# Performance work log

Measured on AMD Instinct MI355X. Metric: run time of the kernel, lower is better.

## Reference

```python
import jax, jax.numpy as jnp
import numpy as np

N, E, H, L, G = 50000, 500000, 128, 4, 1000
EPS = 1e-7      # GENConv message eps
LN_EPS = 1e-5   # torch LayerNorm default


def setup_inputs() -> dict:
    key = jax.random.key(0)
    ks = jax.random.split(key, 24)
    d = {}
    d["x"] = jax.random.normal(ks[0], (N, 9), jnp.float32)
    d["edge_index"] = jax.random.randint(ks[1], (2, E), 0, N, jnp.int32)
    d["edge_attr"] = jax.random.normal(ks[2], (E, 3), jnp.float32)
    d["batch"] = jnp.sort(jax.random.randint(ks[3], (N,), 0, G, jnp.int32))
    s9, s3, sh, s2h = 1/np.sqrt(9), 1/np.sqrt(3), 1/np.sqrt(H), 1/np.sqrt(2*H)
    u = lambda k, shp, s: jax.random.uniform(k, shp, jnp.float32, -s, s)
    d["enc_node_W"] = u(ks[4], (9, H), s9)
    d["enc_node_b"] = u(ks[5], (H,), s9)
    d["enc_edge_W"] = u(ks[6], (3, H), s3)
    d["enc_edge_b"] = u(ks[7], (H,), s3)
    d["ln_g"] = jnp.ones((L, H), jnp.float32)   # DeepGCNLayer pre-norm affine
    d["ln_b"] = jnp.zeros((L, H), jnp.float32)
    d["W1"] = u(ks[8], (L, H, 2*H), sh)          # GENConv MLP layer 1
    d["b1"] = u(ks[9], (L, 2*H), sh)
    d["mlp_ln_g"] = jnp.ones((L, 2*H), jnp.float32)
    d["mlp_ln_b"] = jnp.zeros((L, 2*H), jnp.float32)
    d["W2"] = u(ks[10], (L, 2*H, H), s2h)        # GENConv MLP layer 2
    d["b2"] = u(ks[11], (L, H), s2h)
    d["t"] = jnp.ones((L,), jnp.float32)         # learnable softmax temperature, init 1.0
    return d


def layernorm(x, g, b):
    mu = x.mean(-1, keepdims=True)
    var = ((x - mu) ** 2).mean(-1, keepdims=True)
    return (x - mu) / jnp.sqrt(var + LN_EPS) * g + b


def genconv(h, src, dst, ea, t, W1, b1, lg, lb, W2, b2):
    # message: relu(x_j + edge_attr) + eps   -> [E, H]
    msg = jax.nn.relu(h[src] + ea) + EPS
    # softmax aggregation over incoming edges, per channel
    logits = t * msg
    m = jax.ops.segment_max(logits, dst, num_segments=N)
    num = jnp.exp(logits - m[dst])
    den = jax.ops.segment_sum(num, dst, num_segments=N)
    alpha = num / den[dst]
    agg = jax.ops.segment_sum(msg * alpha, dst, num_segments=N)
    out = agg + h  # root residual inside GENConv
    z = jax.nn.relu(layernorm(out @ W1 + b1, lg, lb))
    return z @ W2 + b2


def reference(x, edge_index, edge_attr, batch, enc_node_W, enc_node_b,
              enc_edge_W, enc_edge_b, ln_g, ln_b, W1, b1, mlp_ln_g, mlp_ln_b,
              W2, b2, t):
    src, dst = edge_index[0], edge_index[1]
    h = x @ enc_node_W + enc_node_b            # node encoder  [N, H]
    ea = edge_attr @ enc_edge_W + enc_edge_b   # edge encoder  [E, H]
    # layer 0: conv only (DeeperGCN forward uses layers[0].conv directly)
    h = genconv(h, src, dst, ea, t[0], W1[0], b1[0], mlp_ln_g[0], mlp_ln_b[0], W2[0], b2[0])
    # layers 1..L-1: res+ block: x + conv(relu(LN(x))); dropout is identity (eval)
    for i in range(1, L):
        z = jax.nn.relu(layernorm(h, ln_g[i], ln_b[i]))
        h = h + genconv(z, src, dst, ea, t[i], W1[i], b1[i], mlp_ln_g[i], mlp_ln_b[i], W2[i], b2[i])
    h = jax.nn.relu(layernorm(h, ln_g[0], ln_b[0]))  # reuses layer-0 norm
    # global mean pool over graphs
    counts = jax.ops.segment_sum(jnp.ones((N,), h.dtype), batch, num_segments=G)
    sums = jax.ops.segment_sum(h, batch, num_segments=G)
    return sums / jnp.maximum(counts, 1.0)[:, None]
```

## Files before the change

### kernel.cpp

```cpp
#include <hip/hip_runtime.h>

#define NN 50000
#define NE 500000
#define HD 128
#define HD2 256
#define NL 4
#define NG 1000

constexpr float MSG_EPS = 1e-7f;
constexpr float LNEPS   = 1e-5f;

typedef float  f32x4  __attribute__((ext_vector_type(4)));
typedef __bf16 bf16x8 __attribute__((ext_vector_type(8)));

__device__ __forceinline__ unsigned short f2b(float f) {
    unsigned int u = __float_as_uint(f);
    unsigned int r = u + 0x7FFFu + ((u >> 16) & 1u);
    return (unsigned short)(r >> 16);
}
__device__ __forceinline__ float b2f(unsigned short h) {
    return __uint_as_float(((unsigned int)h) << 16);
}
__device__ __forceinline__ unsigned int pack2(float a, float b) {
    return (unsigned int)f2b(a) | ((unsigned int)f2b(b) << 16);
}

__global__ void k_encode_nodes(const float* __restrict__ x, const float* __restrict__ W,
                               const float* __restrict__ b, unsigned short* __restrict__ zb) {
    int n = blockIdx.x;
    int c = threadIdx.x;
    float xr[9];
#pragma unroll
    for (int k = 0; k < 9; k++) xr[k] = x[n * 9 + k];
    float acc = b[c];
#pragma unroll
    for (int k = 0; k < 9; k++) acc = fmaf(xr[k], W[k * HD + c], acc);
    zb[n * HD + c] = f2b(acc);
}

__global__ void k_prep(const float* __restrict__ W1, const float* __restrict__ W2,
                       unsigned short* __restrict__ W1T, unsigned short* __restrict__ W2T) {
    int idx = blockIdx.x * 256 + threadIdx.x;
    {
        int k = idx & 127, n = (idx >> 7) & 255, l = idx >> 15;
        W1T[idx] = f2b(W1[(l * 128 + k) * 256 + n]);
    }
    {
        int k = idx & 255, n = (idx >> 8) & 127, l = idx >> 15;
        W2T[idx] = f2b(W2[(l * 256 + k) * 128 + n]);
    }
}

__global__ void k_hist(const int* __restrict__ dst, int* __restrict__ counts) {
    int e = blockIdx.x * blockDim.x + threadIdx.x;
    if (e < NE) atomicAdd(&counts[dst[e]], 1);
}

#define SCAN_B 512
__global__ void k_scan1(const int* __restrict__ counts, int* __restrict__ incl,
                        int* __restrict__ bsum) {
    __shared__ int s[SCAN_B];
    int i = blockIdx.x * SCAN_B + threadIdx.x;
    int v = (i < NN) ? counts[i] : 0;
    s[threadIdx.x] = v;
    __syncthreads();
    for (int off = 1; off < SCAN_B; off <<= 1) {
        int t = (threadIdx.x >= off) ? s[threadIdx.x - off] : 0;
        __syncthreads();
        s[threadIdx.x] += t;
        __syncthreads();
    }
    if (i < NN) incl[i] = s[threadIdx.x];
    if (threadIdx.x == SCAN_B - 1) bsum[blockIdx.x] = s[threadIdx.x];
}

__global__ void k_scan2(const int* __restrict__ bsum, int* __restrict__ boff, int nb) {
    __shared__ int s[128];
    int v = (threadIdx.x < nb) ? bsum[threadIdx.x] : 0;
    s[threadIdx.x] = v;
    __syncthreads();
    for (int off = 1; off < 128; off <<= 1) {
        int t = (threadIdx.x >= off) ? s[threadIdx.x - off] : 0;
        __syncthreads();
        s[threadIdx.x] += t;
        __syncthreads();
    }
    if (threadIdx.x < nb) boff[threadIdx.x] = s[threadIdx.x] - v;
}

__global__ void k_scan3(const int* __restrict__ incl, const int* __restrict__ boff,
                        int* __restrict__ row_start) {
    int i = blockIdx.x * SCAN_B + threadIdx.x;
    if (i < NN) row_start[i + 1] = incl[i] + boff[blockIdx.x];
    if (i == 0) row_start[0] = 0;
}

__global__ void k_scatter(const int* __restrict__ src, const int* __restrict__ dst,
                          const float* __restrict__ eattr, const int* __restrict__ row_start,
                          int* __restrict__ cursor, float4* __restrict__ aperm) {
    int e = blockIdx.x * blockDim.x + threadIdx.x;
    if (e >= NE) return;
    int d = dst[e];
    int p = row_start[d] + atomicAdd(&cursor[d], 1);
    float4 v;
    v.x = eattr[e * 3 + 0];
    v.y = eattr[e * 3 + 1];
    v.z = eattr[e * 3 + 2];
    v.w = __int_as_float(src[e]);
    aperm[p] = v;
}

__device__ __forceinline__ void edge_acc2(float4 a, unsigned int zz, float2 w0, float2 w1,
                                          float2 w2, float2 bb, float tv, float& num0,
                                          float& num1, float& wm0, float& wm1) {
    float zx = b2f((unsigned short)zz), zy = b2f((unsigned short)(zz >> 16));
    float eax = fmaf(a.x, w0.x, fmaf(a.y, w1.x, fmaf(a.z, w2.x, bb.x)));
    float eay = fmaf(a.x, w0.y, fmaf(a.y, w1.y, fmaf(a.z, w2.y, bb.y)));
    float mx = fmaxf(zx + eax, 0.f) + MSG_EPS;
    float my = fmaxf(zy + eay, 0.f) + MSG_EPS;
    float ex = __expf(tv * mx), ey = __expf(tv * my);
    num0 += ex;
    num1 += ey;
    wm0 = fmaf(mx, ex, wm0);
    wm1 = fmaf(my, ey, wm1);
}

#define AGG_CHUNKS_R ((((NN + 31) / 32) + 7) / 8 * 8)
#define AGG_BLOCKS (AGG_CHUNKS_R * 8)
__global__ __launch_bounds__(256) void k_aggregate(const unsigned short* __restrict__ zbin,
                                                   const float4* __restrict__ aperm,
                                                   const int* __restrict__ row_start,
                                                   const float* __restrict__ We,
                                                   const float* __restrict__ be,
                                                   const float* __restrict__ t, int layer,
                                                   unsigned int* __restrict__ outb) {
    int w = threadIdx.x >> 6, lane = threadIdx.x & 63;
    int bid = blockIdx.x;
    int jj = bid >> 3;
    int chunk = (bid & 7) + ((jj >> 3) << 3);
    int n = chunk * 32 + (jj & 7) * 4 + w;
    if (n >= NN) return;
    int c = lane * 2;
    float2 w0 = *(const float2*)&We[c];
    float2 w1 = *(const float2*)&We[HD + c];
    float2 w2 = *(const float2*)&We[2 * HD + c];
    float2 bb = *(const float2*)&be[c];
    float tv = t[layer];
    int s0 = row_start[n], s1 = row_start[n + 1];
    float num0 = 0.f, num1 = 0.f, wm0 = 0.f, wm1 = 0.f;
    const unsigned int* z32 = (const unsigned int*)zbin;
    int p = s0;
    for (; p + 4 <= s1; p += 4) {
        float4 a0 = aperm[p], a1 = aperm[p + 1], a2 = aperm[p + 2], a3 = aperm[p + 3];
        unsigned int zz0 = z32[(size_t)__float_as_int(a0.w) * 64 + lane];
        unsigned int zz1 = z32[(size_t)__float_as_int(a1.w) * 64 + lane];
        unsigned int zz2 = z32[(size_t)__float_as_int(a2.w) * 64 + lane];
        unsigned int zz3 = z32[(size_t)__float_as_int(a3.w) * 64 + lane];
        edge_acc2(a0, zz0, w0, w1, w2, bb, tv, num0, num1, wm0, wm1);
        edge_acc2(a1, zz1, w0, w1, w2, bb, tv, num0, num1, wm0, wm1);
        edge_acc2(a2, zz2, w0, w1, w2, bb, tv, num0, num1, wm0, wm1);
        edge_acc2(a3, zz3, w0, w1, w2, bb, tv, num0, num1, wm0, wm1);
    }
    for (; p < s1; p++) {
        float4 a = aperm[p];
        unsigned int zz = z32[(size_t)__float_as_int(a.w) * 64 + lane];
        edge_acc2(a, zz, w0, w1, w2, bb, tv, num0, num1, wm0, wm1);
    }
    unsigned int zn = z32[(size_t)n * 64 + lane];
    float ox = ((s1 > s0) ? (wm0 / num0) : 0.f) + b2f((unsigned short)zn);
    float oy = ((s1 > s0) ? (wm1 / num1) : 0.f) + b2f((unsigned short)(zn >> 16));
    outb[(size_t)n * 64 + lane] = pack2(ox, oy);
}

#define BM 32
#define HS_LD 264
#define HT_LD 136

__global__ __launch_bounds__(256) void k_mlp(const unsigned short* __restrict__ outb,
                                             const unsigned short* __restrict__ W1T,
                                             const float* __restrict__ b1l,
                                             const float* __restrict__ lgl,
                                             const float* __restrict__ lbl,
                                             const unsigned short* __restrict__ W2T,
                                             const float* __restrict__ b2l,
                                             unsigned short* __restrict__ h,
                                             const float* __restrict__ gn,
                                             const float* __restrict__ bn,
                                             unsigned short* __restrict__ zb,
                                             int add_residual, int store_h) {
    __shared__ __align__(16) unsigned short Hs[BM * HS_LD];
    __shared__ __align__(16) unsigned short Ht[BM * HT_LD];
    __shared__ __align__(16) float2 st1[2][16][4];

    int nb = blockIdx.x * BM;
    int tid = threadIdx.x;
    int w = tid >> 6, lane = tid & 63, q = lane >> 4, i = lane & 15;

    unsigned int hv[8];
    const unsigned int* h32c = (const unsigned int*)h;
    if (add_residual) {
#pragma unroll
        for (int it = 0; it < 8; it++) {
            int row = nb + w + it * 4;
            hv[it] = (row < NN) ? h32c[(size_t)row * 64 + lane] : 0u;
        }
    } else {
#pragma unroll
        for (int it = 0; it < 8; it++) hv[it] = 0u;
    }
    float2 gg = *(const float2*)&gn[lane * 2];
    float2 cc = *(const float2*)&bn[lane * 2];

    f32x4 acc[2][4];
#pragma unroll
    for (int rt = 0; rt < 2; rt++)
#pragma unroll
        for (int ct = 0; ct < 4; ct++) acc[rt][ct] = (f32x4){0.f, 0.f, 0.f, 0.f};

    bf16x8 acur[2], bcur[4];
#pragma unroll
    for (int rt = 0; rt < 2; rt++) {
        int row = nb + rt * 16 + i;
        acur[rt] = (row < NN) ? *(const bf16x8*)&outb[(size_t)row * HD + q * 8]
                              : (bf16x8)(__bf16)0.f;
    }
#pragma unroll
    for (int ct = 0; ct < 4; ct++)
        bcur[ct] = *(const bf16x8*)&W1T[(w * 64 + ct * 16 + i) * HD + q * 8];

#pragma unroll
    for (int ks = 0; ks < 4; ks++) {
        bf16x8 anxt[2], bnxt[4];
        if (ks < 3) {
#pragma unroll
            for (int rt = 0; rt < 2; rt++) {
                int row = nb + rt * 16 + i;
                anxt[rt] = (row < NN)
                               ? *(const bf16x8*)&outb[(size_t)row * HD + (ks + 1) * 32 + q * 8]
                               : (bf16x8)(__bf16)0.f;
            }
#pragma unroll
            for (int ct = 0; ct < 4; ct++)
                bnxt[ct] =
                    *(const bf16x8*)&W1T[(w * 64 + ct * 16 + i) * HD + (ks + 1) * 32 + q * 8];
        }
#pragma unroll
        for (int rt = 0; rt < 2; rt++)
#pragma unroll
            for (int ct = 0; ct < 4; ct++)
                acc[rt][ct] =
                    __builtin_amdgcn_mfma_f32_16x16x32_bf16(acur[rt], bcur[ct], acc[rt][ct],
                                                            0, 0, 0);
        if (ks < 3) {
#pragma unroll
            for (int rt = 0; rt < 2; rt++) acur[rt] = anxt[rt];
#pragma unroll
            for (int ct = 0; ct < 4; ct++) bcur[ct] = bnxt[ct];
        }
    }

#pragma unroll
    for (int ct = 0; ct < 4; ct++) {
        float bb = b1l[w * 64 + ct * 16 + i];
#pragma unroll
        for (int rt = 0; rt < 2; rt++)
#pragma unroll
            for (int r = 0; r < 4; r++) acc[rt][ct][r] += bb;
    }

    {
        float sv[2][4], qv[2][4];
#pragma unroll
        for (int rt = 0; rt < 2; rt++)
#pragma unroll
            for (int r = 0; r < 4; r++) {
                float s = acc[rt][0][r] + acc[rt][1][r] + acc[rt][2][r] + acc[rt][3][r];
                float sq = 0.f;
#pragma unroll
                for (int ct = 0; ct < 4; ct++) sq = fmaf(acc[rt][ct][r], acc[rt][ct][r], sq);
                sv[rt][r] = s;
                qv[rt][r] = sq;
            }
#pragma unroll
        for (int m = 1; m <= 8; m <<= 1)
#pragma unroll
            for (int rt = 0; rt < 2; rt++)
#pragma unroll
                for (int r = 0; r < 4; r++) {
                    sv[rt][r] += __shfl_xor(sv[rt][r], m);
                    qv[rt][r] += __shfl_xor(qv[rt][r], m);
                }
        if (i == 0) {
#pragma unroll
            for (int rt = 0; rt < 2; rt++)
#pragma unroll
                for (int r = 0; r < 4; r++)
                    st1[rt][q * 4 + r][w] = make_float2(sv[rt][r], qv[rt][r]);
        }
    }
    __syncthreads();

    {
        float mu[2][4], inv[2][4];
#pragma unroll
        for (int rt = 0; rt < 2; rt++)
#pragma unroll
            for (int r = 0; r < 4; r++) {
                const float4* sp = (const float4*)&st1[rt][q * 4 + r][0];
                float4 a = sp[0], b = sp[1];
                float S = a.x + a.z + b.x + b.z;
                float Q = a.y + a.w + b.y + b.w;
                float m_ = S * (1.f / 256.f);
                float v_ = Q * (1.f / 256.f) - m_ * m_;
                mu[rt][r] = m_;
                inv[rt][r] = rsqrtf(v_ + LNEPS);
            }
#pragma unroll
        for (int ct = 0; ct < 4; ct++) {
            float g = lgl[w * 64 + ct * 16 + i];
            float c = lbl[w * 64 + ct * 16 + i];
#pragma unroll
            for (int rt = 0; rt < 2; rt++)
#pragma unroll
                for (int r = 0; r < 4; r++) {
                    float v =
                        fmaxf(fmaf((acc[rt][ct][r] - mu[rt][r]) * inv[rt][r], g, c), 0.f);
                    Hs[(rt * 16 + q * 4 + r) * HS_LD + w * 64 + ct * 16 + i] = f2b(v);
                }
        }
    }
    __syncthreads();

    f32x4 acc2[2][2];
#pragma unroll
    for (int rt = 0; rt < 2; rt++)
#pragma unroll
        for (int ct = 0; ct < 2; ct++) acc2[rt][ct] = (f32x4){0.f, 0.f, 0.f, 0.f};

    bf16x8 hc[2], bc[2];
#pragma unroll
    for (int rt = 0; rt < 2; rt++) hc[rt] = *(const bf16x8*)&Hs[(rt * 16 + i) * HS_LD + q * 8];
#pragma unroll
    for (int ct = 0; ct < 2; ct++)
        bc[ct] = *(const bf16x8*)&W2T[(w * 32 + ct * 16 + i) * HD2 + q * 8];

#pragma unroll
    for (int ks = 0; ks < 8; ks++) {
        bf16x8 hn[2], bn2[2];
        if (ks < 7) {
#pragma unroll
            for (int rt = 0; rt < 2; rt++)
                hn[rt] = *(const bf16x8*)&Hs[(rt * 16 + i) * HS_LD + (ks + 1) * 32 + q * 8];
#pragma unroll
            for (int ct = 0; ct < 2; ct++)
                bn2[ct] =
                    *(const bf16x8*)&W2T[(w * 32 + ct * 16 + i) * HD2 + (ks + 1) * 32 + q * 8];
        }
#pragma unroll
        for (int rt = 0; rt < 2; rt++)
#pragma unroll
            for (int ct = 0; ct < 2; ct++)
                acc2[rt][ct] = __builtin_amdgcn_mfma_f32_16x16x32_bf16(hc[rt], bc[ct],
                                                                      acc2[rt][ct], 0, 0, 0);
        if (ks < 7) {
#pragma unroll
            for (int rt = 0; rt < 2; rt++) hc[rt] = hn[rt];
#pragma unroll
            for (int ct = 0; ct < 2; ct++) bc[ct] = bn2[ct];
        }
    }

#pragma unroll
    for (int ct = 0; ct < 2; ct++) {
        float bb = b2l[w * 32 + ct * 16 + i];
#pragma unroll
        for (int rt = 0; rt < 2; rt++)
#pragma unroll
            for (int r = 0; r < 4; r++)
                Ht[(rt * 16 + q * 4 + r) * HT_LD + w * 32 + ct * 16 + i] =
                    f2b(acc2[rt][ct][r] + bb);
    }
    __syncthreads();

    {
        const unsigned int* Ht32 = (const unsigned int*)Ht;
        unsigned int* h32 = (unsigned int*)h;
        unsigned int* zb32 = (unsigned int*)zb;
#pragma unroll
        for (int it = 0; it < 8; it++) {
            int rr = w + it * 4;
            int row = nb + rr;
            unsigned int tv = Ht32[rr * (HT_LD / 2) + lane];
            float cx = b2f((unsigned short)tv) + b2f((unsigned short)hv[it]);
            float cy = b2f((unsigned short)(tv >> 16)) + b2f((unsigned short)(hv[it] >> 16));
            float s = cx + cy, sq = cx * cx + cy * cy;
#pragma unroll
            for (int m = 32; m >= 1; m >>= 1) {
                s += __shfl_xor(s, m);
                sq += __shfl_xor(sq, m);
            }
            float mu = s * (1.f / 128.f);
            float var = sq * (1.f / 128.f) - mu * mu;
            float inv = rsqrtf(var + LNEPS);
            float z0 = fmaxf(fmaf((cx - mu) * inv, gg.x, cc.x), 0.f);
            float z1 = fmaxf(fmaf((cy - mu) * inv, gg.y, cc.y), 0.f);
            if (row < NN) {
                if (store_h) h32[(size_t)row * 64 + lane] = pack2(cx, cy);
                zb32[(size_t)row * 64 + lane] = pack2(z0, z1);
            }
        }
    }
}

__global__ void k_gbounds(const int* __restrict__ batch, int* __restrict__ gstart) {
    int g = blockIdx.x * blockDim.x + threadIdx.x;
    if (g > NG) return;
    int lo = 0, hi = NN;
    while (lo < hi) {
        int mid = (lo + hi) >> 1;
        if (batch[mid] < g) lo = mid + 1;
        else hi = mid;
    }
    gstart[g] = lo;
}

__global__ void k_pool(const unsigned short* __restrict__ zb, const int* __restrict__ gstart,
                       float* __restrict__ out) {
    int g = blockIdx.x;
    int c = threadIdx.x;
    int a = gstart[g], b = gstart[g + 1];
    float s0 = 0.f, s1 = 0.f;
    int n = a;
    for (; n + 2 <= b; n += 2) {
        s0 += b2f(zb[(size_t)n * HD + c]);
        s1 += b2f(zb[(size_t)(n + 1) * HD + c]);
    }
    if (n < b) s0 += b2f(zb[(size_t)n * HD + c]);
    out[g * HD + c] = (s0 + s1) / fmaxf((float)(b - a), 1.f);
}

extern "C" void kernel_launch(void* const* d_in, const int* in_sizes, int n_in, void* d_out,
                              int out_size, void* d_ws, size_t ws_size, hipStream_t stream) {
    const float* x     = (const float*)d_in[0];
    const int* ei      = (const int*)d_in[1];
    const float* eattr = (const float*)d_in[2];
    const int* batch   = (const int*)d_in[3];
    const float* encW  = (const float*)d_in[4];
    const float* encB  = (const float*)d_in[5];
    const float* eW    = (const float*)d_in[6];
    const float* eB    = (const float*)d_in[7];
    const float* ln_g  = (const float*)d_in[8];
    const float* ln_b  = (const float*)d_in[9];
    const float* W1    = (const float*)d_in[10];
    const float* b1    = (const float*)d_in[11];
    const float* mlg   = (const float*)d_in[12];
    const float* mlb   = (const float*)d_in[13];
    const float* W2    = (const float*)d_in[14];
    const float* b2    = (const float*)d_in[15];
    const float* t     = (const float*)d_in[16];
    const int* src = ei;
    const int* dst = ei + NE;

    char* w = (char*)d_ws;
    auto alloc = [&](size_t bytes) {
        char* p = w;
        w += (bytes + 255) & ~size_t(255);
        return p;
    };
    unsigned short* h    = (unsigned short*)alloc(sizeof(unsigned short) * NN * HD);
    unsigned short* zb   = (unsigned short*)alloc(sizeof(unsigned short) * NN * HD);
    unsigned int* outb   = (unsigned int*)alloc(sizeof(unsigned int) * NN * HD / 2);
    float4* aperm        = (float4*)alloc(sizeof(float4) * NE);
    int* row_start       = (int*)alloc(sizeof(int) * (NN + 1));
    int* counts          = (int*)alloc(sizeof(int) * NN);
    int* cursor          = (int*)alloc(sizeof(int) * NN);
    int* incl            = (int*)alloc(sizeof(int) * NN);
    int* bsum            = (int*)alloc(sizeof(int) * 128);
    int* boff            = (int*)alloc(sizeof(int) * 128);
    int* gstart          = (int*)alloc(sizeof(int) * (NG + 1));
    unsigned short* W1T  = (unsigned short*)alloc(sizeof(unsigned short) * NL * HD * HD2);
    unsigned short* W2T  = (unsigned short*)alloc(sizeof(unsigned short) * NL * HD2 * HD);

    hipMemsetAsync(counts, 0, sizeof(int) * NN, stream);
    hipMemsetAsync(cursor, 0, sizeof(int) * NN, stream);

    k_prep<<<512, 256, 0, stream>>>(W1, W2, W1T, W2T);
    k_encode_nodes<<<NN, HD, 0, stream>>>(x, encW, encB, zb);
    k_hist<<<(NE + 255) / 256, 256, 0, stream>>>(dst, counts);
    int nsb = (NN + SCAN_B - 1) / SCAN_B;
    k_scan1<<<nsb, SCAN_B, 0, stream>>>(counts, incl, bsum);
    k_scan2<<<1, 128, 0, stream>>>(bsum, boff, nsb);
    k_scan3<<<nsb, SCAN_B, 0, stream>>>(incl, boff, row_start);
    k_scatter<<<(NE + 255) / 256, 256, 0, stream>>>(src, dst, eattr, row_start, cursor, aperm);
    k_gbounds<<<(NG + 256) / 256, 256, 0, stream>>>(batch, gstart);

    for (int l = 0; l < NL; l++) {
        k_aggregate<<<AGG_BLOCKS, 256, 0, stream>>>(zb, aperm, row_start, eW, eB, t, l, outb);
        int ln_next = (l + 1) % NL;
        k_mlp<<<(NN + BM - 1) / BM, 256, 0, stream>>>(
            (const unsigned short*)outb, W1T + (size_t)l * HD * HD2, b1 + l * HD2,
            mlg + l * HD2, mlb + l * HD2, W2T + (size_t)l * HD2 * HD, b2 + l * HD, h,
            ln_g + ln_next * HD, ln_b + ln_next * HD, zb, l > 0, l < NL - 1);
    }
    k_pool<<<NG, HD, 0, stream>>>(zb, gstart, (float*)d_out);
}
```

Baseline: 508.2 us.

## Fuse edge aggregation into MLP kernel with ping-pong z buffers

Merges the separate aggregation kernel into the per-layer MLP kernel. Each block now aggregates its 32 nodes, interleaving two nodes per wave to raise memory-level parallelism, and writes the results into a swizzled LDS tile that feeds the MFMA A operand. This removes the global round-trip of the aggregated tensor and one launch per layer. Since the fused kernel reads z from neighbours while other blocks write the next z, z is now ping-ponged between two buffers. In exchange the block count drops to N/32 with uneven per-block gather work, and the GEMM waits on the slowest aggregation wave.

After: 613.3 us. +20.7%, slower.

```diff
diff --git a/kernel.cpp b/kernel.cpp
--- a/kernel.cpp
+++ b/kernel.cpp
@@ -125,71 +125,22 @@
     wm1 = fmaf(my, ey, wm1);
 }
 
-#define AGG_CHUNKS_R ((((NN + 31) / 32) + 7) / 8 * 8)
-#define AGG_BLOCKS (AGG_CHUNKS_R * 8)
-__global__ __launch_bounds__(256) void k_aggregate(const unsigned short* __restrict__ zbin,
-                                                   const float4* __restrict__ aperm,
-                                                   const int* __restrict__ row_start,
-                                                   const float* __restrict__ We,
-                                                   const float* __restrict__ be,
-                                                   const float* __restrict__ t, int layer,
-                                                   unsigned int* __restrict__ outb) {
-    int w = threadIdx.x >> 6, lane = threadIdx.x & 63;
-    int bid = blockIdx.x;
-    int jj = bid >> 3;
-    int chunk = (bid & 7) + ((jj >> 3) << 3);
-    int n = chunk * 32 + (jj & 7) * 4 + w;
-    if (n >= NN) return;
-    int c = lane * 2;
-    float2 w0 = *(const float2*)&We[c];
-    float2 w1 = *(const float2*)&We[HD + c];
-    float2 w2 = *(const float2*)&We[2 * HD + c];
-    float2 bb = *(const float2*)&be[c];
-    float tv = t[layer];
-    int s0 = row_start[n], s1 = row_start[n + 1];
-    float num0 = 0.f, num1 = 0.f, wm0 = 0.f, wm1 = 0.f;
-    const unsigned int* z32 = (const unsigned int*)zbin;
-    int p = s0;
-    for (; p + 4 <= s1; p += 4) {
-        float4 a0 = aperm[p], a1 = aperm[p + 1], a2 = aperm[p + 2], a3 = aperm[p + 3];
-        unsigned int zz0 = z32[(size_t)__float_as_int(a0.w) * 64 + lane];
-        unsigned int zz1 = z32[(size_t)__float_as_int(a1.w) * 64 + lane];
-        unsigned int zz2 = z32[(size_t)__float_as_int(a2.w) * 64 + lane];
-        unsigned int zz3 = z32[(size_t)__float_as_int(a3.w) * 64 + lane];
-        edge_acc2(a0, zz0, w0, w1, w2, bb, tv, num0, num1, wm0, wm1);
-        edge_acc2(a1, zz1, w0, w1, w2, bb, tv, num0, num1, wm0, wm1);
-        edge_acc2(a2, zz2, w0, w1, w2, bb, tv, num0, num1, wm0, wm1);
-        edge_acc2(a3, zz3, w0, w1, w2, bb, tv, num0, num1, wm0, wm1);
-    }
-    for (; p < s1; p++) {
-        float4 a = aperm[p];
-        unsigned int zz = z32[(size_t)__float_as_int(a.w) * 64 + lane];
-        edge_acc2(a, zz, w0, w1, w2, bb, tv, num0, num1, wm0, wm1);
-    }
-    unsigned int zn = z32[(size_t)n * 64 + lane];
-    float ox = ((s1 > s0) ? (wm0 / num0) : 0.f) + b2f((unsigned short)zn);
-    float oy = ((s1 > s0) ? (wm1 / num1) : 0.f) + b2f((unsigned short)(zn >> 16));
-    outb[(size_t)n * 64 + lane] = pack2(ox, oy);
-}
-
 #define BM 32
 #define HS_LD 264
-#define HT_LD 136
-
-__global__ __launch_bounds__(256) void k_mlp(const unsigned short* __restrict__ outb,
-                                             const unsigned short* __restrict__ W1T,
-                                             const float* __restrict__ b1l,
-                                             const float* __restrict__ lgl,
-                                             const float* __restrict__ lbl,
-                                             const unsigned short* __restrict__ W2T,
-                                             const float* __restrict__ b2l,
-                                             unsigned short* __restrict__ h,
-                                             const float* __restrict__ gn,
-                                             const float* __restrict__ bn,
-                                             unsigned short* __restrict__ zb,
-                                             int add_residual, int store_h) {
+#define AS_W 68
+
+__global__ __launch_bounds__(256) void k_layer(
+    const unsigned short* __restrict__ zin, const float4* __restrict__ aperm,
+    const int* __restrict__ row_start, const float* __restrict__ We,
+    const float* __restrict__ be, const float* __restrict__ t, int layer,
+    const unsigned short* __restrict__ W1T, const float* __restrict__ b1l,
+    const float* __restrict__ lgl, const float* __restrict__ lbl,
+    const unsigned short* __restrict__ W2T, const float* __restrict__ b2l,
+    unsigned short* __restrict__ h, const float* __restrict__ gn,
+    const float* __restrict__ bn, unsigned short* __restrict__ zout,
+    int add_residual, int store_h) {
     __shared__ __align__(16) unsigned short Hs[BM * HS_LD];
-    __shared__ __align__(16) unsigned short Ht[BM * HT_LD];
+    __shared__ __align__(16) unsigned int AsHt[BM * AS_W];
     __shared__ __align__(16) float2 st1[2][16][4];
 
     int nb = blockIdx.x * BM;
@@ -211,49 +162,133 @@
     float2 gg = *(const float2*)&gn[lane * 2];
     float2 cc = *(const float2*)&bn[lane * 2];
 
+    {
+        int c = lane * 2;
+        float2 w0 = *(const float2*)&We[c];
+        float2 w1 = *(const float2*)&We[HD + c];
+        float2 w2 = *(const float2*)&We[2 * HD + c];
+        float2 bb = *(const float2*)&be[c];
+        float tv = t[layer];
+        const unsigned int* z32 = (const unsigned int*)zin;
+
+#pragma unroll
+        for (int m = 0; m < 4; m++) {
+            int rrA = w + 8 * m, rrB = rrA + 4;
+            int nA = nb + rrA, nB = nb + rrB;
+            int sA0 = 0, sA1 = 0, sB0 = 0, sB1 = 0;
+            if (nA < NN) { sA0 = row_start[nA]; sA1 = row_start[nA + 1]; }
+            if (nB < NN) { sB0 = row_start[nB]; sB1 = row_start[nB + 1]; }
+            float numA0 = 0.f, numA1 = 0.f, wmA0 = 0.f, wmA1 = 0.f;
+            float numB0 = 0.f, numB1 = 0.f, wmB0 = 0.f, wmB1 = 0.f;
+            int pa = sA0, pb = sB0;
+            while (pa + 2 <= sA1 && pb + 2 <= sB1) {
+                float4 eA0 = aperm[pa], eA1 = aperm[pa + 1];
+                float4 eB0 = aperm[pb], eB1 = aperm[pb + 1];
+                unsigned int gA0 = z32[(size_t)__float_as_int(eA0.w) * 64 + lane];
+                unsigned int gA1 = z32[(size_t)__float_as_int(eA1.w) * 64 + lane];
+                unsigned int gB0 = z32[(size_t)__float_as_int(eB0.w) * 64 + lane];
+                unsigned int gB1 = z32[(size_t)__float_as_int(eB1.w) * 64 + lane];
+                edge_acc2(eA0, gA0, w0, w1, w2, bb, tv, numA0, numA1, wmA0, wmA1);
+                edge_acc2(eA1, gA1, w0, w1, w2, bb, tv, numA0, numA1, wmA0, wmA1);
+                edge_acc2(eB0, gB0, w0, w1, w2, bb, tv, numB0, numB1, wmB0, wmB1);
+                edge_acc2(eB1, gB1, w0, w1, w2, bb, tv, numB0, numB1, wmB0, wmB1);
+                pa += 2;
+                pb += 2;
+            }
+            for (; pa + 4 <= sA1; pa += 4) {
+                float4 e0 = aperm[pa], e1 = aperm[pa + 1], e2 = aperm[pa + 2],
+                       e3 = aperm[pa + 3];
+                unsigned int g0 = z32[(size_t)__float_as_int(e0.w) * 64 + lane];
+                unsigned int g1 = z32[(size_t)__float_as_int(e1.w) * 64 + lane];
+                unsigned int g2 = z32[(size_t)__float_as_int(e2.w) * 64 + lane];
+                unsigned int g3 = z32[(size_t)__float_as_int(e3.w) * 64 + lane];
+                edge_acc2(e0, g0, w0, w1, w2, bb, tv, numA0, numA1, wmA0, wmA1);
+                edge_acc2(e1, g1, w0, w1, w2, bb, tv, numA0, numA1, wmA0, wmA1);
+                edge_acc2(e2, g2, w0, w1, w2, bb, tv, numA0, numA1, wmA0, wmA1);
+                edge_acc2(e3, g3, w0, w1, w2, bb, tv, numA0, numA1, wmA0, wmA1);
+            }
+            for (; pa < sA1; pa++) {
+                float4 e0 = aperm[pa];
+                unsigned int g0 = z32[(size_t)__float_as_int(e0.w) * 64 + lane];
+                edge_acc2(e0, g0, w0, w1, w2, bb, tv, numA0, numA1, wmA0, wmA1);
+            }
+            for (; pb + 4 <= sB1; pb += 4) {
+                float4 e0 = aperm[pb], e1 = aperm[pb + 1], e2 = aperm[pb + 2],
+                       e3 = aperm[pb + 3];
+                unsigned int g0 = z32[(size_t)__float_as_int(e0.w) * 64 + lane];
+                unsigned int g1 = z32[(size_t)__float_as_int(e1.w) * 64 + lane];
+                unsigned int g2 = z32[(size_t)__float_as_int(e2.w) * 64 + lane];
+                unsigned int g3 = z32[(size_t)__float_as_int(e3.w) * 64 + lane];
+                edge_acc2(e0, g0, w0, w1, w2, bb, tv, numB0, numB1, wmB0, wmB1);
+                edge_acc2(e1, g1, w0, w1, w2, bb, tv, numB0, numB1, wmB0, wmB1);
+                edge_acc2(e2, g2, w0, w1, w2, bb, tv, numB0, numB1, wmB0, wmB1);
+                edge_acc2(e3, g3, w0, w1, w2, bb, tv, numB0, numB1, wmB0, wmB1);
+            }
+            for (; pb < sB1; pb++) {
+                float4 e0 = aperm[pb];
+                unsigned int g0 = z32[(size_t)__float_as_int(e0.w) * 64 + lane];
+                edge_acc2(e0, g0, w0, w1, w2, bb, tv, numB0, numB1, wmB0, wmB1);
+            }
+            {
+                unsigned int vA = 0u, vB = 0u;
+                if (nA < NN) {
+                    unsigned int zn = z32[(size_t)nA * 64 + lane];
+                    float ox = ((sA1 > sA0) ? (wmA0 / numA0) : 0.f) + b2f((unsigned short)zn);
+                    float oy =
+                        ((sA1 > sA0) ? (wmA1 / numA1) : 0.f) + b2f((unsigned short)(zn >> 16));
+                    vA = pack2(ox, oy);
+                }
+                if (nB < NN) {
+                    unsigned int zn = z32[(size_t)nB * 64 + lane];
+                    float ox = ((sB1 > sB0) ? (wmB0 / numB0) : 0.f) + b2f((unsigned short)zn);
+                    float oy =
+                        ((sB1 > sB0) ? (wmB1 / numB1) : 0.f) + b2f((unsigned short)(zn >> 16));
+                    vB = pack2(ox, oy);
+                }
+                AsHt[rrA * AS_W + (lane ^ ((rrA & 7) << 2))] = vA;
+                AsHt[rrB * AS_W + (lane ^ ((rrB & 7) << 2))] = vB;
+            }
+        }
+    }
+    __syncthreads();
+
     f32x4 acc[2][4];
 #pragma unroll
     for (int rt = 0; rt < 2; rt++)
 #pragma unroll
         for (int ct = 0; ct < 4; ct++) acc[rt][ct] = (f32x4){0.f, 0.f, 0.f, 0.f};
 
-    bf16x8 acur[2], bcur[4];
-#pragma unroll
-    for (int rt = 0; rt < 2; rt++) {
-        int row = nb + rt * 16 + i;
-        acur[rt] = (row < NN) ? *(const bf16x8*)&outb[(size_t)row * HD + q * 8]
-                              : (bf16x8)(__bf16)0.f;
-    }
+    bf16x8 bcur[4];
 #pragma unroll
     for (int ct = 0; ct < 4; ct++)
         bcur[ct] = *(const bf16x8*)&W1T[(w * 64 + ct * 16 + i) * HD + q * 8];
 
+    int sw = (i & 7) << 2;
 #pragma unroll
     for (int ks = 0; ks < 4; ks++) {
-        bf16x8 anxt[2], bnxt[4];
+        bf16x8 bnxt[4];
         if (ks < 3) {
-#pragma unroll
-            for (int rt = 0; rt < 2; rt++) {
-                int row = nb + rt * 16 + i;
-                anxt[rt] = (row < NN)
-                               ? *(const bf16x8*)&outb[(size_t)row * HD + (ks + 1) * 32 + q * 8]
-                               : (bf16x8)(__bf16)0.f;
-            }
 #pragma unroll
             for (int ct = 0; ct < 4; ct++)
                 bnxt[ct] =
                     *(const bf16x8*)&W1T[(w * 64 + ct * 16 + i) * HD + (ks + 1) * 32 + q * 8];
         }
+        bf16x8 av[2];
+#pragma unroll
+        for (int rt = 0; rt < 2; rt++) {
+            int rr = rt * 16 + i;
+            const char* p =
+                (const char*)AsHt + rr * (AS_W * 4) + (((ks * 16 + q * 4) ^ sw) << 2);
+            av[rt] = *(const bf16x8*)p;
+        }
 #pragma unroll
         for (int rt = 0; rt < 2; rt++)
 #pragma unroll
             for (int ct = 0; ct < 4; ct++)
                 acc[rt][ct] =
-                    __builtin_amdgcn_mfma_f32_16x16x32_bf16(acur[rt], bcur[ct], acc[rt][ct],
+                    __builtin_amdgcn_mfma_f32_16x16x32_bf16(av[rt], bcur[ct], acc[rt][ct],
                                                             0, 0, 0);
         if (ks < 3) {
-#pragma unroll
-            for (int rt = 0; rt < 2; rt++) acur[rt] = anxt[rt];
 #pragma unroll
             for (int ct = 0; ct < 4; ct++) bcur[ct] = bnxt[ct];
         }
@@ -370,27 +405,30 @@
         }
     }
 
-#pragma unroll
-    for (int ct = 0; ct < 2; ct++) {
-        float bb = b2l[w * 32 + ct * 16 + i];
-#pragma unroll
-        for (int rt = 0; rt < 2; rt++)
-#pragma unroll
-            for (int r = 0; r < 4; r++)
-                Ht[(rt * 16 + q * 4 + r) * HT_LD + w * 32 + ct * 16 + i] =
-                    f2b(acc2[rt][ct][r] + bb);
+    {
+        unsigned short* Ht = (unsigned short*)AsHt;
+#pragma unroll
+        for (int ct = 0; ct < 2; ct++) {
+            float bb = b2l[w * 32 + ct * 16 + i];
+#pragma unroll
+            for (int rt = 0; rt < 2; rt++)
+#pragma unroll
+                for (int r = 0; r < 4; r++)
+                    Ht[(rt * 16 + q * 4 + r) * (2 * AS_W) + w * 32 + ct * 16 + i] =
+                        f2b(acc2[rt][ct][r] + bb);
+        }
     }
     __syncthreads();
 
     {
-        const unsigned int* Ht32 = (const unsigned int*)Ht;
+        const unsigned int* Ht32 = AsHt;
         unsigned int* h32 = (unsigned int*)h;
-        unsigned int* zb32 = (unsigned int*)zb;
+        unsigned int* zb32 = (unsigned int*)zout;
 #pragma unroll
         for (int it = 0; it < 8; it++) {
             int rr = w + it * 4;
             int row = nb + rr;
-            unsigned int tv = Ht32[rr * (HT_LD / 2) + lane];
+            unsigned int tv = Ht32[rr * AS_W + lane];
             float cx = b2f((unsigned short)tv) + b2f((unsigned short)hv[it]);
             float cy = b2f((unsigned short)(tv >> 16)) + b2f((unsigned short)(hv[it] >> 16));
             float s = cx + cy, sq = cx * cx + cy * cy;
@@ -468,8 +506,8 @@
         return p;
     };
     unsigned short* h    = (unsigned short*)alloc(sizeof(unsigned short) * NN * HD);
-    unsigned short* zb   = (unsigned short*)alloc(sizeof(unsigned short) * NN * HD);
-    unsigned int* outb   = (unsigned int*)alloc(sizeof(unsigned int) * NN * HD / 2);
+    unsigned short* zbA  = (unsigned short*)alloc(sizeof(unsigned short) * NN * HD);
+    unsigned short* zbB  = (unsigned short*)alloc(sizeof(unsigned short) * NN * HD);
     float4* aperm        = (float4*)alloc(sizeof(float4) * NE);
     int* row_start       = (int*)alloc(sizeof(int) * (NN + 1));
     int* counts          = (int*)alloc(sizeof(int) * NN);
@@ -485,7 +523,7 @@
     hipMemsetAsync(cursor, 0, sizeof(int) * NN, stream);
 
     k_prep<<<512, 256, 0, stream>>>(W1, W2, W1T, W2T);
-    k_encode_nodes<<<NN, HD, 0, stream>>>(x, encW, encB, zb);
+    k_encode_nodes<<<NN, HD, 0, stream>>>(x, encW, encB, zbA);
     k_hist<<<(NE + 255) / 256, 256, 0, stream>>>(dst, counts);
     int nsb = (NN + SCAN_B - 1) / SCAN_B;
     k_scan1<<<nsb, SCAN_B, 0, stream>>>(counts, incl, bsum);
@@ -494,13 +532,15 @@
     k_scatter<<<(NE + 255) / 256, 256, 0, stream>>>(src, dst, eattr, row_start, cursor, aperm);
     k_gbounds<<<(NG + 256) / 256, 256, 0, stream>>>(batch, gstart);
 
+    int nblk = (NN + BM - 1) / BM;
     for (int l = 0; l < NL; l++) {
-        k_aggregate<<<AGG_BLOCKS, 256, 0, stream>>>(zb, aperm, row_start, eW, eB, t, l, outb);
+        const unsigned short* zin = (l & 1) ? zbB : zbA;
+        unsigned short* zout      = (l & 1) ? zbA : zbB;
         int ln_next = (l + 1) % NL;
-        k_mlp<<<(NN + BM - 1) / BM, 256, 0, stream>>>(
-            (const unsigned short*)outb, W1T + (size_t)l * HD * HD2, b1 + l * HD2,
+        k_layer<<<nblk, 256, 0, stream>>>(
+            zin, aperm, row_start, eW, eB, t, l, W1T + (size_t)l * HD * HD2, b1 + l * HD2,
             mlg + l * HD2, mlb + l * HD2, W2T + (size_t)l * HD2 * HD, b2 + l * HD, h,
-            ln_g + ln_next * HD, ln_b + ln_next * HD, zb, l > 0, l < NL - 1);
-    }
-    k_pool<<<NG, HD, 0, stream>>>(zb, gstart, (float*)d_out);
-}
+            ln_g + ln_next * HD, ln_b + ln_next * HD, zout, l > 0, l < NL - 1);
+    }
+    k_pool<<<NG, HD, 0, stream>>>(zbA, gstart, (float*)d_out);
+}
```

## Software-pipeline edge loads in aggregate, prescale src indices, preload MLP A tiles

Applied to the files above, without the earlier changes.

The scatter kernel now stores each source index pre-multiplied by 64, so the aggregate gather can use a 32-bit add instead of a 64-bit multiply. The aggregate loop is software-pipelined so the next four edge records load while the current four gathers are processed, and the self-row load is issued early. The swizzled block-to-node mapping is dropped in favour of a linear one. In the MLP kernel all A-operand fragments are loaded up front rather than double-buffered, which raises register pressure in exchange for more memory-level parallelism.

Result: faster. 490.3 us (-3.5%).

```diff
diff --git a/kernel.cpp b/kernel.cpp
--- a/kernel.cpp
+++ b/kernel.cpp
@@ -106,7 +106,7 @@
     v.x = eattr[e * 3 + 0];
     v.y = eattr[e * 3 + 1];
     v.z = eattr[e * 3 + 2];
-    v.w = __int_as_float(src[e]);
+    v.w = __int_as_float(src[e] << 6);
     aperm[p] = v;
 }
 
@@ -125,8 +125,6 @@
     wm1 = fmaf(my, ey, wm1);
 }
 
-#define AGG_CHUNKS_R ((((NN + 31) / 32) + 7) / 8 * 8)
-#define AGG_BLOCKS (AGG_CHUNKS_R * 8)
 __global__ __launch_bounds__(256) void k_aggregate(const unsigned short* __restrict__ zbin,
                                                    const float4* __restrict__ aperm,
                                                    const int* __restrict__ row_start,
@@ -135,10 +133,7 @@
                                                    const float* __restrict__ t, int layer,
                                                    unsigned int* __restrict__ outb) {
     int w = threadIdx.x >> 6, lane = threadIdx.x & 63;
-    int bid = blockIdx.x;
-    int jj = bid >> 3;
-    int chunk = (bid & 7) + ((jj >> 3) << 3);
-    int n = chunk * 32 + (jj & 7) * 4 + w;
+    int n = blockIdx.x * 4 + w;
     if (n >= NN) return;
     int c = lane * 2;
     float2 w0 = *(const float2*)&We[c];
@@ -147,26 +142,45 @@
     float2 bb = *(const float2*)&be[c];
     float tv = t[layer];
     int s0 = row_start[n], s1 = row_start[n + 1];
+    const unsigned int* z32 = (const unsigned int*)zbin;
+    unsigned int zn = z32[(size_t)n * 64 + lane];
     float num0 = 0.f, num1 = 0.f, wm0 = 0.f, wm1 = 0.f;
-    const unsigned int* z32 = (const unsigned int*)zbin;
     int p = s0;
-    for (; p + 4 <= s1; p += 4) {
-        float4 a0 = aperm[p], a1 = aperm[p + 1], a2 = aperm[p + 2], a3 = aperm[p + 3];
-        unsigned int zz0 = z32[(size_t)__float_as_int(a0.w) * 64 + lane];
-        unsigned int zz1 = z32[(size_t)__float_as_int(a1.w) * 64 + lane];
-        unsigned int zz2 = z32[(size_t)__float_as_int(a2.w) * 64 + lane];
-        unsigned int zz3 = z32[(size_t)__float_as_int(a3.w) * 64 + lane];
-        edge_acc2(a0, zz0, w0, w1, w2, bb, tv, num0, num1, wm0, wm1);
-        edge_acc2(a1, zz1, w0, w1, w2, bb, tv, num0, num1, wm0, wm1);
-        edge_acc2(a2, zz2, w0, w1, w2, bb, tv, num0, num1, wm0, wm1);
-        edge_acc2(a3, zz3, w0, w1, w2, bb, tv, num0, num1, wm0, wm1);
+    if (p + 4 <= s1) {
+        float4 A0 = aperm[p], A1 = aperm[p + 1], A2 = aperm[p + 2], A3 = aperm[p + 3];
+        for (; p + 8 <= s1; p += 4) {
+            unsigned int g0 = z32[(unsigned int)__float_as_int(A0.w) + lane];
+            unsigned int g1 = z32[(unsigned int)__float_as_int(A1.w) + lane];
+            unsigned int g2 = z32[(unsigned int)__float_as_int(A2.w) + lane];
+            unsigned int g3 = z32[(unsigned int)__float_as_int(A3.w) + lane];
+            float4 B0 = aperm[p + 4], B1 = aperm[p + 5], B2 = aperm[p + 6],
+                   B3 = aperm[p + 7];
+            edge_acc2(A0, g0, w0, w1, w2, bb, tv, num0, num1, wm0, wm1);
+            edge_acc2(A1, g1, w0, w1, w2, bb, tv, num0, num1, wm0, wm1);
+            edge_acc2(A2, g2, w0, w1, w2, bb, tv, num0, num1, wm0, wm1);
+            edge_acc2(A3, g3, w0, w1, w2, bb, tv, num0, num1, wm0, wm1);
+            A0 = B0;
+            A1 = B1;
+            A2 = B2;
+            A3 = B3;
+        }
+        {
+            unsigned int g0 = z32[(unsigned int)__float_as_int(A0.w) + lane];
+            unsigned int g1 = z32[(unsigned int)__float_as_int(A1.w) + lane];
+            unsigned int g2 = z32[(unsigned int)__float_as_int(A2.w) + lane];
+            unsigned int g3 = z32[(unsigned int)__float_as_int(A3.w) + lane];
+            edge_acc2(A0, g0, w0, w1, w2, bb, tv, num0, num1, wm0, wm1);
+            edge_acc2(A1, g1, w0, w1, w2, bb, tv, num0, num1, wm0, wm1);
+            edge_acc2(A2, g2, w0, w1, w2, bb, tv, num0, num1, wm0, wm1);
+            edge_acc2(A3, g3, w0, w1, w2, bb, tv, num0, num1, wm0, wm1);
+            p += 4;
+        }
     }
     for (; p < s1; p++) {
         float4 a = aperm[p];
-        unsigned int zz = z32[(size_t)__float_as_int(a.w) * 64 + lane];
+        unsigned int zz = z32[(unsigned int)__float_as_int(a.w) + lane];
         edge_acc2(a, zz, w0, w1, w2, bb, tv, num0, num1, wm0, wm1);
     }
-    unsigned int zn = z32[(size_t)n * 64 + lane];
     float ox = ((s1 > s0) ? (wm0 / num0) : 0.f) + b2f((unsigned short)zn);
     float oy = ((s1 > s0) ? (wm1 / num1) : 0.f) + b2f((unsigned short)(zn >> 16));
     outb[(size_t)n * 64 + lane] = pack2(ox, oy);
@@ -196,6 +210,17 @@
     int tid = threadIdx.x;
     int w = tid >> 6, lane = tid & 63, q = lane >> 4, i = lane & 15;
 
+    bf16x8 areg[2][4];
+#pragma unroll
+    for (int rt = 0; rt < 2; rt++) {
+        int row = nb + rt * 16 + i;
+#pragma unroll
+        for (int ks = 0; ks < 4; ks++)
+            areg[rt][ks] = (row < NN)
+                               ? *(const bf16x8*)&outb[(size_t)row * HD + ks * 32 + q * 8]
+                               : (bf16x8)(__bf16)0.f;
+    }
+
     unsigned int hv[8];
     const unsigned int* h32c = (const unsigned int*)h;
     if (add_residual) {
@@ -217,28 +242,15 @@
 #pragma unroll
         for (int ct = 0; ct < 4; ct++) acc[rt][ct] = (f32x4){0.f, 0.f, 0.f, 0.f};
 
-    bf16x8 acur[2], bcur[4];
-#pragma unroll
-    for (int rt = 0; rt < 2; rt++) {
-        int row = nb + rt * 16 + i;
-        acur[rt] = (row < NN) ? *(const bf16x8*)&outb[(size_t)row * HD + q * 8]
-                              : (bf16x8)(__bf16)0.f;
-    }
+    bf16x8 bcur[4];
 #pragma unroll
     for (int ct = 0; ct < 4; ct++)
         bcur[ct] = *(const bf16x8*)&W1T[(w * 64 + ct * 16 + i) * HD + q * 8];
 
 #pragma unroll
     for (int ks = 0; ks < 4; ks++) {
-        bf16x8 anxt[2], bnxt[4];
+        bf16x8 bnxt[4];
         if (ks < 3) {
-#pragma unroll
-            for (int rt = 0; rt < 2; rt++) {
-                int row = nb + rt * 16 + i;
-                anxt[rt] = (row < NN)
-                               ? *(const bf16x8*)&outb[(size_t)row * HD + (ks + 1) * 32 + q * 8]
-                               : (bf16x8)(__bf16)0.f;
-            }
 #pragma unroll
             for (int ct = 0; ct < 4; ct++)
                 bnxt[ct] =
@@ -248,12 +260,9 @@
         for (int rt = 0; rt < 2; rt++)
 #pragma unroll
             for (int ct = 0; ct < 4; ct++)
-                acc[rt][ct] =
-                    __builtin_amdgcn_mfma_f32_16x16x32_bf16(acur[rt], bcur[ct], acc[rt][ct],
-                                                            0, 0, 0);
+                acc[rt][ct] = __builtin_amdgcn_mfma_f32_16x16x32_bf16(areg[rt][ks], bcur[ct],
+                                                                     acc[rt][ct], 0, 0, 0);
         if (ks < 3) {
-#pragma unroll
-            for (int rt = 0; rt < 2; rt++) acur[rt] = anxt[rt];
 #pragma unroll
             for (int ct = 0; ct < 4; ct++) bcur[ct] = bnxt[ct];
         }
@@ -495,7 +504,7 @@
     k_gbounds<<<(NG + 256) / 256, 256, 0, stream>>>(batch, gstart);
 
     for (int l = 0; l < NL; l++) {
-        k_aggregate<<<AGG_BLOCKS, 256, 0, stream>>>(zb, aperm, row_start, eW, eB, t, l, outb);
+        k_aggregate<<<(NN + 3) / 4, 256, 0, stream>>>(zb, aperm, row_start, eW, eB, t, l, outb);
         int ln_next = (l + 1) % NL;
         k_mlp<<<(NN + BM - 1) / BM, 256, 0, stream>>>(
             (const unsigned short*)outb, W1T + (size_t)l * HD * HD2, b1 + l * HD2,
```
